# Performance work log

Hardware: AMD Instinct MI355X
Metric: run time of the kernel (lower is better)

Reference implementation:

```python
import jax, jax.numpy as jnp
import numpy as np

N0, N1, N2 = 120000, 30000, 6000   # node frontier sizes per hop
E0, E1 = 480000, 96000             # sampled edges per layer (~fanout 16)
D = 128                            # in_channels == hidden_size
R = 8                              # num_relations
NB = 4                             # num_bases
ETOT = 3000000                     # global edge count (edge_type_all)


def setup_inputs() -> dict:
    key = jax.random.key(0)
    ks = jax.random.split(key, 24)
    s = 1.0 / np.sqrt(D)
    f32 = jnp.float32
    inp = {
        "x": jax.random.normal(ks[0], (N0, D), dtype=f32),
        "src0": jax.random.randint(ks[1], (E0,), 0, N0),
        "dst0": jax.random.randint(ks[2], (E0,), 0, N1),
        "e_id0": jax.random.randint(ks[3], (E0,), 0, ETOT),
        "src1": jax.random.randint(ks[4], (E1,), 0, N1),
        "dst1": jax.random.randint(ks[5], (E1,), 0, N2),
        "e_id1": jax.random.randint(ks[6], (E1,), 0, ETOT),
        "edge_type_all": jax.random.randint(ks[7], (ETOT,), 0, R),
        # pre_layer: linear + relu
        "pre_W": jax.random.normal(ks[8], (D, D), dtype=f32) * s,
        "pre_b": jnp.zeros((D,), f32),
        # RGCNConv layer 0 (basis decomposition)
        "basis0": jax.random.normal(ks[9], (NB, D, D), dtype=f32) * s,
        "comp0": jax.random.normal(ks[10], (R, NB), dtype=f32) * (1.0 / np.sqrt(NB)),
        "root0": jax.random.normal(ks[11], (D, D), dtype=f32) * s,
        "bias0": jnp.zeros((D,), f32),
        "g0": jnp.ones((D,), f32),
        "be0": jnp.zeros((D,), f32),
        # RGCNConv layer 1
        "basis1": jax.random.normal(ks[12], (NB, D, D), dtype=f32) * s,
        "comp1": jax.random.normal(ks[13], (R, NB), dtype=f32) * (1.0 / np.sqrt(NB)),
        "root1": jax.random.normal(ks[14], (D, D), dtype=f32) * s,
        "bias1": jnp.zeros((D,), f32),
        "g1": jnp.ones((D,), f32),
        "be1": jnp.zeros((D,), f32),
        # post_layer: single linear
        "post_W": jax.random.normal(ks[15], (D, D), dtype=f32) * s,
        "post_b": jnp.zeros((D,), f32),
    }
    return inp


def _layernorm(x, g, b, eps=1e-5):
    mu = jnp.mean(x, axis=-1, keepdims=True)
    var = jnp.mean(jnp.square(x - mu), axis=-1, keepdims=True)
    return (x - mu) * jax.lax.rsqrt(var + eps) * g + b


def _rgcn_conv(x, n_dst, src, dst, etype, basis, comp, root, bias):
    # Bipartite RGCNConv with basis decomposition and mean aggregation.
    # Since messages W[r] @ x[src] are linear, aggregate per relation first
    # (segment_sum of raw features), then apply the relation weight once.
    x_t = x[:n_dst]                                    # [n_dst, D]
    out = x_t @ root + bias                            # root/self transform
    W = jnp.einsum('rb,bio->rio', comp, basis)         # [R, D, D]
    x_j = x[src]                                       # [E, D] gather
    deg = jax.ops.segment_sum(jnp.ones(src.shape[0], x.dtype), dst,
                              num_segments=n_dst)      # mean over all relations
    agg = jnp.zeros((n_dst, W.shape[-1]), x.dtype)
    for r in range(W.shape[0]):                        # R=8 structurally distinct
        m = (etype == r).astype(x.dtype)[:, None]
        s_r = jax.ops.segment_sum(x_j * m, dst, num_segments=n_dst)
        agg = agg + s_r @ W[r]
    return out + agg / jnp.maximum(deg, 1.0)[:, None]


def reference(x, src0, dst0, e_id0, src1, dst1, e_id1, edge_type_all,
              pre_W, pre_b, basis0, comp0, root0, bias0, g0, be0,
              basis1, comp1, root1, bias1, g1, be1, post_W, post_b):
    # pre_layer: linear + relu (GeneralMultiLayer, final_act=True)
    h = jax.nn.relu(x @ pre_W + pre_b)
    # layer 0: edge-type gather -> relational conv -> norm -> act (eval: no dropout)
    h = _rgcn_conv(h, N1, src0, dst0, edge_type_all[e_id0],
                   basis0, comp0, root0, bias0)
    h = jax.nn.relu(_layernorm(h, g0, be0))
    # layer 1
    h = _rgcn_conv(h, N2, src1, dst1, edge_type_all[e_id1],
                   basis1, comp1, root1, bias1)
    h = jax.nn.relu(_layernorm(h, g1, be1))
    # post_layer: single linear MLP
    return h @ post_W + post_b
```

## Files before the change

### kernel.cpp

```cpp
#include <hip/hip_runtime.h>
#include <cstdint>

#define DD 128
#define CAP 64
#define ESB 128
#define E0C 480000
#define E1C 96000
#define N0C 120000
#define N1C 30000
#define N2C 6000
#define ETOTC 3000000

typedef unsigned short u16;
typedef __attribute__((ext_vector_type(8))) short bf16x8;
typedef __attribute__((ext_vector_type(16))) float f32x16;

__device__ __forceinline__ u16 f2b(float f) {
    union { float f; unsigned u; } a; a.f = f;
    unsigned r = (a.u + 0x7fffu + ((a.u >> 16) & 1u)) >> 16;
    return (u16)r;
}
__device__ __forceinline__ float b2f(u16 u) {
    union { unsigned u; float f; } a; a.u = ((unsigned)u) << 16;
    return a.f;
}

struct WtJob { const float* src[12]; };
__global__ __launch_bounds__(256) void prep_kernel(
    WtJob job, u16* __restrict__ dst, int* __restrict__ cnt0, int* __restrict__ cnt1,
    const int* __restrict__ etype, unsigned* __restrict__ r4)
{
    int gtid = blockIdx.x * 256 + threadIdx.x;
    for (int i = gtid; i < N1C + N2C; i += 256 * 256) {
        if (i < N1C) cnt0[i] = 0; else cnt1[i - N1C] = 0;
    }
    for (int i = gtid; i < ETOTC / 8; i += 256 * 256) {
        int4 a = ((const int4*)etype)[i * 2];
        int4 b = ((const int4*)etype)[i * 2 + 1];
        unsigned p = (unsigned)(a.x & 7) | ((unsigned)(a.y & 7) << 4)
                   | ((unsigned)(a.z & 7) << 8) | ((unsigned)(a.w & 7) << 12)
                   | ((unsigned)(b.x & 7) << 16) | ((unsigned)(b.y & 7) << 20)
                   | ((unsigned)(b.z & 7) << 24) | ((unsigned)(b.w & 7) << 28);
        r4[i] = p;
    }
    if (blockIdx.x >= 192) return;
    __shared__ float tile[32][33];
    int m = blockIdx.x >> 4;
    int t4 = blockIdx.x & 15;
    int tr = (t4 >> 2) * 32;
    int tc = (t4 & 3) * 32;
    int lx = threadIdx.x & 31, ly = threadIdx.x >> 5;
    #pragma unroll
    for (int yy = 0; yy < 32; yy += 8)
        tile[ly + yy][lx] = job.src[m][(tr + ly + yy) * DD + tc + lx];
    __syncthreads();
    int tid = threadIdx.x;
    if (tid < 128) {
        int nl = tid >> 2, kch = tid & 3;
        int k = tr + kch * 8, n = tc + nl;
        int kc = k >> 4, half = (k >> 3) & 1;
        int t = n >> 5, l31 = n & 31;
        bf16x8 pk;
        #pragma unroll
        for (int j = 0; j < 8; ++j) pk[j] = (short)f2b(tile[kch * 8 + j][nl]);
        *(bf16x8*)(dst + (size_t)m * 16384 + kc * 2048 + t * 512 + half * 256 + l31 * 8) = pk;
    }
}

__global__ __launch_bounds__(256) void fillpre_kernel(
    const float* __restrict__ x,
    const int* __restrict__ src0, const int* __restrict__ dst0, const int* __restrict__ eid0,
    const int* __restrict__ src1, const int* __restrict__ dst1, const int* __restrict__ eid1,
    const unsigned* __restrict__ r4,
    int* __restrict__ cnt0, int* __restrict__ cnt1,
    int* __restrict__ ep0, int* __restrict__ ep1,
    const u16* __restrict__ Wr, const float* __restrict__ bias,
    u16* __restrict__ h0)
{
    if (blockIdx.x < ESB) {
        const int STR = ESB * 256;
        int gtid = blockIdx.x * 256 + threadIdx.x;
        int e = gtid;
        for (; e + 3 * STR < E0C + E1C; e += 4 * STR) {
            int d[4], eidv[4], s[4], r[4], pos[4];
            bool L0[4];
            #pragma unroll
            for (int u = 0; u < 4; ++u) {
                int idx = e + u * STR;
                L0[u] = idx < E0C;
                int ee = L0[u] ? idx : idx - E0C;
                d[u]    = L0[u] ? dst0[ee] : dst1[ee];
                eidv[u] = L0[u] ? eid0[ee] : eid1[ee];
                s[u]    = L0[u] ? src0[ee] : src1[ee];
            }
            #pragma unroll
            for (int u = 0; u < 4; ++u)
                r[u] = (int)((r4[eidv[u] >> 3] >> ((eidv[u] & 7) << 2)) & 7u);
            #pragma unroll
            for (int u = 0; u < 4; ++u)
                pos[u] = atomicAdd(L0[u] ? &cnt0[d[u]] : &cnt1[d[u]], 1);
            #pragma unroll
            for (int u = 0; u < 4; ++u) {
                if (pos[u] < CAP) {
                    int* ep = L0[u] ? ep0 : ep1;
                    ep[(size_t)d[u] * CAP + pos[u]] = s[u] | (r[u] << 28);
                }
            }
        }
        for (; e < E0C + E1C; e += STR) {
            bool L0 = e < E0C;
            int ee = L0 ? e : e - E0C;
            int d   = L0 ? dst0[ee] : dst1[ee];
            int eid = L0 ? eid0[ee] : eid1[ee];
            int s   = L0 ? src0[ee] : src1[ee];
            int r = (int)((r4[eid >> 3] >> ((eid & 7) << 2)) & 7u);
            int pos = atomicAdd(L0 ? &cnt0[d] : &cnt1[d], 1);
            if (pos < CAP) (L0 ? ep0 : ep1)[(size_t)d * CAP + pos] = s | (r << 28);
        }
        return;
    }

    int bid = blockIdx.x - ESB;
    int wave = threadIdx.x >> 6;
    int lane = threadIdx.x & 63;
    int l31 = lane & 31, half = lane >> 5;
    int m0 = (bid * 4 + wave) * 32;
    if (m0 >= N0C) return;
    int arow = m0 + l31;
    bool rv = arow < N0C;

    const float* Aq = x + (size_t)arow * DD;
    float4 st[16];
    if (rv) {
        #pragma unroll
        for (int c = 0; c < 16; ++c)
            st[c] = *(const float4*)(Aq + ((c >> 1) * 16 + half * 8) + (c & 1) * 4);
    } else {
        #pragma unroll
        for (int c = 0; c < 16; ++c) st[c] = make_float4(0.f, 0.f, 0.f, 0.f);
    }
    f32x16 accs[4];
    #pragma unroll
    for (int t = 0; t < 4; ++t)
        #pragma unroll
        for (int i = 0; i < 16; ++i) accs[t][i] = 0.f;
    #pragma unroll
    for (int kc = 0; kc < 8; ++kc) {
        bf16x8 bfr[4];
        #pragma unroll
        for (int t = 0; t < 4; ++t)
            bfr[t] = *(const bf16x8*)(Wr + (size_t)((kc * 4 + t) * 64 + lane) * 8);
        float4 u0 = st[2 * kc], u1 = st[2 * kc + 1];
        bf16x8 af;
        af[0] = (short)f2b(u0.x); af[1] = (short)f2b(u0.y);
        af[2] = (short)f2b(u0.z); af[3] = (short)f2b(u0.w);
        af[4] = (short)f2b(u1.x); af[5] = (short)f2b(u1.y);
        af[6] = (short)f2b(u1.z); af[7] = (short)f2b(u1.w);
        #pragma unroll
        for (int t = 0; t < 4; ++t)
            accs[t] = __builtin_amdgcn_mfma_f32_32x32x16_bf16(af, bfr[t], accs[t], 0, 0, 0);
    }
    float bb[4];
    #pragma unroll
    for (int t = 0; t < 4; ++t) bb[t] = bias[t * 32 + l31];
    #pragma unroll
    for (int reg = 0; reg < 16; ++reg) {
        int rl = (reg & 3) + 8 * (reg >> 2) + 4 * half;
        int row = m0 + rl;
        if (row < N0C) {
            #pragma unroll
            for (int t = 0; t < 4; ++t)
                h0[(size_t)row * DD + t * 32 + l31] =
                    f2b(fmaxf(accs[t][reg] + bb[t], 0.f));
        }
    }
}

__global__ __launch_bounds__(256) void agg_kernel(
    const u16* __restrict__ h, const int* __restrict__ cnt,
    const int* __restrict__ ep, const float* __restrict__ comp,
    u16* __restrict__ T, int ndst)
{
    __shared__ float4 cmp4[8];
    if (threadIdx.x < 8) cmp4[threadIdx.x] = ((const float4*)comp)[threadIdx.x];
    __syncthreads();
    int row = blockIdx.x * 4 + (threadIdx.x >> 6);
    if (row >= ndst) return;
    int lane = threadIdx.x & 63;
    int n = cnt[row];
    int end = n < CAP ? n : CAP;
    const int* erow = ep + (size_t)row * CAP;
    float a0[4] = {0.f, 0.f, 0.f, 0.f};
    float a1[4] = {0.f, 0.f, 0.f, 0.f};
    int j = 0;
    for (; j + 16 <= end; j += 16) {
        int vv[16]; unsigned gg[16];
        #pragma unroll
        for (int u = 0; u < 16; ++u) vv[u] = erow[j + u];
        #pragma unroll
        for (int u = 0; u < 16; ++u)
            gg[u] = *(const unsigned*)(h + (size_t)(vv[u] & 0x0FFFFFFF) * DD + 2 * lane);
        #pragma unroll
        for (int u = 0; u < 16; ++u) {
            float4 c = cmp4[vv[u] >> 28];
            float x0 = b2f((u16)(gg[u] & 0xffffu));
            float x1 = b2f((u16)(gg[u] >> 16));
            a0[0] = fmaf(c.x, x0, a0[0]); a1[0] = fmaf(c.x, x1, a1[0]);
            a0[1] = fmaf(c.y, x0, a0[1]); a1[1] = fmaf(c.y, x1, a1[1]);
            a0[2] = fmaf(c.z, x0, a0[2]); a1[2] = fmaf(c.z, x1, a1[2]);
            a0[3] = fmaf(c.w, x0, a0[3]); a1[3] = fmaf(c.w, x1, a1[3]);
        }
    }
    for (; j + 4 <= end; j += 4) {
        int vv[4]; unsigned gg[4];
        #pragma unroll
        for (int u = 0; u < 4; ++u) vv[u] = erow[j + u];
        #pragma unroll
        for (int u = 0; u < 4; ++u)
            gg[u] = *(const unsigned*)(h + (size_t)(vv[u] & 0x0FFFFFFF) * DD + 2 * lane);
        #pragma unroll
        for (int u = 0; u < 4; ++u) {
            float4 c = cmp4[vv[u] >> 28];
            float x0 = b2f((u16)(gg[u] & 0xffffu));
            float x1 = b2f((u16)(gg[u] >> 16));
            a0[0] = fmaf(c.x, x0, a0[0]); a1[0] = fmaf(c.x, x1, a1[0]);
            a0[1] = fmaf(c.y, x0, a0[1]); a1[1] = fmaf(c.y, x1, a1[1]);
            a0[2] = fmaf(c.z, x0, a0[2]); a1[2] = fmaf(c.z, x1, a1[2]);
            a0[3] = fmaf(c.w, x0, a0[3]); a1[3] = fmaf(c.w, x1, a1[3]);
        }
    }
    for (; j < end; ++j) {
        int v = erow[j];
        unsigned g = *(const unsigned*)(h + (size_t)(v & 0x0FFFFFFF) * DD + 2 * lane);
        float4 c = cmp4[v >> 28];
        float x0 = b2f((u16)(g & 0xffffu));
        float x1 = b2f((u16)(g >> 16));
        a0[0] = fmaf(c.x, x0, a0[0]); a1[0] = fmaf(c.x, x1, a1[0]);
        a0[1] = fmaf(c.y, x0, a0[1]); a1[1] = fmaf(c.y, x1, a1[1]);
        a0[2] = fmaf(c.z, x0, a0[2]); a1[2] = fmaf(c.z, x1, a1[2]);
        a0[3] = fmaf(c.w, x0, a0[3]); a1[3] = fmaf(c.w, x1, a1[3]);
    }
    float inv = 1.f / fmaxf((float)n, 1.f);
    #pragma unroll
    for (int b = 0; b < 4; ++b) {
        unsigned pk = (unsigned)f2b(a0[b] * inv) | ((unsigned)f2b(a1[b] * inv) << 16);
        *(unsigned*)(T + ((size_t)b * ndst + row) * DD + 2 * lane) = pk;
    }
}

__global__ __launch_bounds__(64) void mfma_gemm_ln(
    const u16* __restrict__ Ap, const u16* __restrict__ Ar,
    const u16* __restrict__ Wp, const u16* __restrict__ Wr,
    const float* __restrict__ bias, const float* __restrict__ gw,
    const float* __restrict__ bw, u16* __restrict__ Cv, int nrows)
{
    int lane = threadIdx.x & 63;
    int l31 = lane & 31, half = lane >> 5;
    int m0 = blockIdx.x * 32;
    int arow = m0 + l31;
    bool rv = arow < nrows;
    f32x16 acc[4];
    #pragma unroll
    for (int t = 0; t < 4; ++t)
        #pragma unroll
        for (int i = 0; i < 16; ++i) acc[t][i] = 0.f;

    bf16x8 A0[8], A1[8];
    if (rv) {
        #pragma unroll
        for (int c = 0; c < 8; ++c)
            A0[c] = *(const bf16x8*)(Ap + (size_t)arow * DD + c * 16 + half * 8);
    } else {
        #pragma unroll
        for (int c = 0; c < 8; ++c) A0[c] = (bf16x8){0,0,0,0,0,0,0,0};
    }
    for (int p = 0; p <= 4; ++p) {
        const u16* Wsel = (p == 4) ? Wr : Wp + (size_t)p * 16384;
        if (p < 4) {
            const u16* An = (p + 1 == 4) ? Ar : Ap + (size_t)(p + 1) * nrows * DD;
            if (rv) {
                #pragma unroll
                for (int c = 0; c < 8; ++c)
                    A1[c] = *(const bf16x8*)(An + (size_t)arow * DD + c * 16 + half * 8);
            } else {
                #pragma unroll
                for (int c = 0; c < 8; ++c) A1[c] = (bf16x8){0,0,0,0,0,0,0,0};
            }
        }
        #pragma unroll
        for (int kc = 0; kc < 8; ++kc) {
            bf16x8 bfr[4];
            #pragma unroll
            for (int t = 0; t < 4; ++t)
                bfr[t] = *(const bf16x8*)(Wsel + (size_t)((kc * 4 + t) * 64 + lane) * 8);
            #pragma unroll
            for (int t = 0; t < 4; ++t)
                acc[t] = __builtin_amdgcn_mfma_f32_32x32x16_bf16(A0[kc], bfr[t], acc[t], 0, 0, 0);
        }
        if (p < 4) {
            #pragma unroll
            for (int c = 0; c < 8; ++c) A0[c] = A1[c];
        }
    }

    float bb[4], gg[4], ww[4];
    #pragma unroll
    for (int t = 0; t < 4; ++t) {
        bb[t] = bias[t * 32 + l31];
        gg[t] = gw[t * 32 + l31];
        ww[t] = bw[t * 32 + l31];
    }
    #pragma unroll
    for (int reg = 0; reg < 16; ++reg) {
        int rl = (reg & 3) + 8 * (reg >> 2) + 4 * half;
        int row = m0 + rl;
        float v[4];
        #pragma unroll
        for (int t = 0; t < 4; ++t) v[t] = acc[t][reg] + bb[t];
        float s1 = 0.f, s2 = 0.f;
        #pragma unroll
        for (int t = 0; t < 4; ++t) { s1 += v[t]; s2 += v[t] * v[t]; }
        #pragma unroll
        for (int o = 1; o < 32; o <<= 1) {
            s1 += __shfl_xor(s1, o);
            s2 += __shfl_xor(s2, o);
        }
        float mu = s1 * (1.f / 128.f);
        float var = s2 * (1.f / 128.f) - mu * mu;
        float rstd = rsqrtf(fmaxf(var, 0.f) + 1e-5f);
        if (row < nrows) {
            #pragma unroll
            for (int t = 0; t < 4; ++t)
                Cv[(size_t)row * DD + t * 32 + l31] =
                    f2b(fmaxf((v[t] - mu) * rstd * gg[t] + ww[t], 0.f));
        }
    }
}

__global__ __launch_bounds__(64) void gemm_post_kernel(
    const u16* __restrict__ Ap, const u16* __restrict__ Ar,
    const u16* __restrict__ Wp, const u16* __restrict__ Wr,
    const float* __restrict__ bias, const float* __restrict__ gw,
    const float* __restrict__ bw,
    const u16* __restrict__ Wpost, const float* __restrict__ postb,
    float* __restrict__ outp, int nrows)
{
    __shared__ u16 lt[32][136];
    int lane = threadIdx.x & 63;
    int l31 = lane & 31, half = lane >> 5;
    int m0 = blockIdx.x * 32;
    int arow = m0 + l31;
    bool rv = arow < nrows;
    f32x16 acc[4];
    #pragma unroll
    for (int t = 0; t < 4; ++t)
        #pragma unroll
        for (int i = 0; i < 16; ++i) acc[t][i] = 0.f;

    bf16x8 A0[8], A1[8];
    if (rv) {
        #pragma unroll
        for (int c = 0; c < 8; ++c)
            A0[c] = *(const bf16x8*)(Ap + (size_t)arow * DD + c * 16 + half * 8);
    } else {
        #pragma unroll
        for (int c = 0; c < 8; ++c) A0[c] = (bf16x8){0,0,0,0,0,0,0,0};
    }
    for (int p = 0; p <= 4; ++p) {
        const u16* Wsel = (p == 4) ? Wr : Wp + (size_t)p * 16384;
        if (p < 4) {
            const u16* An = (p + 1 == 4) ? Ar : Ap + (size_t)(p + 1) * nrows * DD;
            if (rv) {
                #pragma unroll
                for (int c = 0; c < 8; ++c)
                    A1[c] = *(const bf16x8*)(An + (size_t)arow * DD + c * 16 + half * 8);
            } else {
                #pragma unroll
                for (int c = 0; c < 8; ++c) A1[c] = (bf16x8){0,0,0,0,0,0,0,0};
            }
        }
        #pragma unroll
        for (int kc = 0; kc < 8; ++kc) {
            bf16x8 bfr[4];
            #pragma unroll
            for (int t = 0; t < 4; ++t)
                bfr[t] = *(const bf16x8*)(Wsel + (size_t)((kc * 4 + t) * 64 + lane) * 8);
            #pragma unroll
            for (int t = 0; t < 4; ++t)
                acc[t] = __builtin_amdgcn_mfma_f32_32x32x16_bf16(A0[kc], bfr[t], acc[t], 0, 0, 0);
        }
        if (p < 4) {
            #pragma unroll
            for (int c = 0; c < 8; ++c) A0[c] = A1[c];
        }
    }

    float bb[4], gg[4], ww[4];
    #pragma unroll
    for (int t = 0; t < 4; ++t) {
        bb[t] = bias[t * 32 + l31];
        gg[t] = gw[t * 32 + l31];
        ww[t] = bw[t * 32 + l31];
    }
    #pragma unroll
    for (int reg = 0; reg < 16; ++reg) {
        int rl = (reg & 3) + 8 * (reg >> 2) + 4 * half;
        float v[4];
        #pragma unroll
        for (int t = 0; t < 4; ++t) v[t] = acc[t][reg] + bb[t];
        float s1 = 0.f, s2 = 0.f;
        #pragma unroll
        for (int t = 0; t < 4; ++t) { s1 += v[t]; s2 += v[t] * v[t]; }
        #pragma unroll
        for (int o = 1; o < 32; o <<= 1) {
            s1 += __shfl_xor(s1, o);
            s2 += __shfl_xor(s2, o);
        }
        float mu = s1 * (1.f / 128.f);
        float var = s2 * (1.f / 128.f) - mu * mu;
        float rstd = rsqrtf(fmaxf(var, 0.f) + 1e-5f);
        #pragma unroll
        for (int t = 0; t < 4; ++t)
            lt[rl][t * 32 + l31] = f2b(fmaxf((v[t] - mu) * rstd * gg[t] + ww[t], 0.f));
    }
    __syncthreads();

    f32x16 acc2[4];
    #pragma unroll
    for (int t = 0; t < 4; ++t)
        #pragma unroll
        for (int i = 0; i < 16; ++i) acc2[t][i] = 0.f;
    bf16x8 A[8];
    #pragma unroll
    for (int c = 0; c < 8; ++c)
        A[c] = *(const bf16x8*)&lt[l31][c * 16 + half * 8];
    #pragma unroll
    for (int kc = 0; kc < 8; ++kc) {
        bf16x8 bfr[4];
        #pragma unroll
        for (int t = 0; t < 4; ++t)
            bfr[t] = *(const bf16x8*)(Wpost + (size_t)((kc * 4 + t) * 64 + lane) * 8);
        #pragma unroll
        for (int t = 0; t < 4; ++t)
            acc2[t] = __builtin_amdgcn_mfma_f32_32x32x16_bf16(A[kc], bfr[t], acc2[t], 0, 0, 0);
    }
    float pb[4];
    #pragma unroll
    for (int t = 0; t < 4; ++t) pb[t] = postb[t * 32 + l31];
    #pragma unroll
    for (int reg = 0; reg < 16; ++reg) {
        int rl = (reg & 3) + 8 * (reg >> 2) + 4 * half;
        int row = m0 + rl;
        if (row < nrows) {
            #pragma unroll
            for (int t = 0; t < 4; ++t)
                outp[(size_t)row * DD + t * 32 + l31] = acc2[t][reg] + pb[t];
        }
    }
}

extern "C" void kernel_launch(void* const* d_in, const int* in_sizes, int n_in,
                              void* d_out, int out_size, void* d_ws, size_t ws_size,
                              hipStream_t stream)
{
    const float* x     = (const float*)d_in[0];
    const int* src0    = (const int*)d_in[1];
    const int* dst0    = (const int*)d_in[2];
    const int* eid0    = (const int*)d_in[3];
    const int* src1    = (const int*)d_in[4];
    const int* dst1    = (const int*)d_in[5];
    const int* eid1    = (const int*)d_in[6];
    const int* etype   = (const int*)d_in[7];
    const float* preW  = (const float*)d_in[8];
    const float* preb  = (const float*)d_in[9];
    const float* basis0 = (const float*)d_in[10];
    const float* comp0  = (const float*)d_in[11];
    const float* root0  = (const float*)d_in[12];
    const float* bias0  = (const float*)d_in[13];
    const float* g0    = (const float*)d_in[14];
    const float* be0   = (const float*)d_in[15];
    const float* basis1 = (const float*)d_in[16];
    const float* comp1  = (const float*)d_in[17];
    const float* root1  = (const float*)d_in[18];
    const float* bias1  = (const float*)d_in[19];
    const float* g1    = (const float*)d_in[20];
    const float* be1   = (const float*)d_in[21];
    const float* postW = (const float*)d_in[22];
    const float* postb = (const float*)d_in[23];
    float* out = (float*)d_out;

    char* ws = (char*)d_ws;
    size_t o = 0;
    auto alloc = [&](size_t bytes) { char* p = ws + o; o += (bytes + 255) & ~(size_t)255; return p; };
    u16* h0   = (u16*)alloc((size_t)N0C * DD * 2);
    u16* T0   = (u16*)alloc((size_t)4 * N1C * DD * 2);
    u16* h1   = (u16*)alloc((size_t)N1C * DD * 2);
    u16* T1   = (u16*)alloc((size_t)4 * N2C * DD * 2);
    u16* wt   = (u16*)alloc((size_t)12 * 16384 * 2);
    int* cnt0 = (int*)alloc((size_t)N1C * 4);
    int* cnt1 = (int*)alloc((size_t)N2C * 4);
    int* ep0  = (int*)alloc((size_t)N1C * CAP * 4);
    int* ep1  = (int*)alloc((size_t)N2C * CAP * 4);
    unsigned* r4 = (unsigned*)alloc((size_t)(ETOTC / 8) * 4);

    WtJob job;
    job.src[0] = preW;
    for (int b = 0; b < 4; ++b) job.src[1 + b] = basis0 + (size_t)b * 16384;
    job.src[5] = root0;
    for (int b = 0; b < 4; ++b) job.src[6 + b] = basis1 + (size_t)b * 16384;
    job.src[10] = root1;
    job.src[11] = postW;

    prep_kernel<<<256, 256, 0, stream>>>(job, wt, cnt0, cnt1, etype, r4);
    fillpre_kernel<<<ESB + (N0C + 127) / 128, 256, 0, stream>>>(
        x, src0, dst0, eid0, src1, dst1, eid1, r4,
        cnt0, cnt1, ep0, ep1, wt + 0 * 16384, preb, h0);
    agg_kernel<<<(N1C + 3) / 4, 256, 0, stream>>>(h0, cnt0, ep0, comp0, T0, N1C);
    mfma_gemm_ln<<<(N1C + 31) / 32, 64, 0, stream>>>(
        T0, h0, wt + 1 * 16384, wt + 5 * 16384, bias0, g0, be0, h1, N1C);
    agg_kernel<<<(N2C + 3) / 4, 256, 0, stream>>>(h1, cnt1, ep1, comp1, T1, N2C);
    gemm_post_kernel<<<(N2C + 31) / 32, 64, 0, stream>>>(
        T1, h1, wt + 6 * 16384, wt + 10 * 16384, bias1, g1, be1,
        wt + 11 * 16384, postb, out, N2C);
}
```

Measured before the change: 274.1 us.

## Fuse the five post-prep stages into one cooperative persistent kernel with grid syncs

Replaces the fillpre, two aggregation and two GEMM launches with a single cooperative kernel of 512 blocks that runs each stage as a grid-strided loop, separated by grid-wide syncs. It targets launch overhead and tail gaps between the dependent stages. In exchange it imposes a fixed grid size on every stage, which may underuse the GPU in the gather-heavy aggregation. It also adds grid barrier costs and replaces a __syncthreads with a waitcnt for the per-wave LDS tile. The original multi-kernel path is kept as a fallback if the cooperative launch fails.

```diff
diff --git a/kernel.cpp b/kernel.cpp
--- a/kernel.cpp
+++ b/kernel.cpp
@@ -1,15 +1,21 @@
 #include <hip/hip_runtime.h>
+#include <hip/hip_cooperative_groups.h>
 #include <cstdint>
+
+namespace cg = cooperative_groups;
 
 #define DD 128
 #define CAP 64
 #define ESB 128
+#define MESB 256
 #define E0C 480000
 #define E1C 96000
 #define N0C 120000
 #define N1C 30000
 #define N2C 6000
 #define ETOTC 3000000
+#define MGB 512
+#define MGW (MGB * 4)
 
 typedef unsigned short u16;
 typedef __attribute__((ext_vector_type(8))) short bf16x8;
@@ -67,78 +73,67 @@
     }
 }
 
-__global__ __launch_bounds__(256) void fillpre_kernel(
-    const float* __restrict__ x,
+
+__device__ __forceinline__ void fill_edges(
+    int nblocks, int blockid,
     const int* __restrict__ src0, const int* __restrict__ dst0, const int* __restrict__ eid0,
     const int* __restrict__ src1, const int* __restrict__ dst1, const int* __restrict__ eid1,
     const unsigned* __restrict__ r4,
     int* __restrict__ cnt0, int* __restrict__ cnt1,
-    int* __restrict__ ep0, int* __restrict__ ep1,
-    const u16* __restrict__ Wr, const float* __restrict__ bias,
-    u16* __restrict__ h0)
-{
-    if (blockIdx.x < ESB) {
-        const int STR = ESB * 256;
-        int gtid = blockIdx.x * 256 + threadIdx.x;
-        int e = gtid;
-        for (; e + 3 * STR < E0C + E1C; e += 4 * STR) {
-            int d[4], eidv[4], s[4], r[4], pos[4];
-            bool L0[4];
-            #pragma unroll
-            for (int u = 0; u < 4; ++u) {
-                int idx = e + u * STR;
-                L0[u] = idx < E0C;
-                int ee = L0[u] ? idx : idx - E0C;
-                d[u]    = L0[u] ? dst0[ee] : dst1[ee];
-                eidv[u] = L0[u] ? eid0[ee] : eid1[ee];
-                s[u]    = L0[u] ? src0[ee] : src1[ee];
+    int* __restrict__ ep0, int* __restrict__ ep1)
+{
+    const int STR = nblocks * 256;
+    int gtid = blockid * 256 + threadIdx.x;
+    int e = gtid;
+    for (; e + 3 * STR < E0C + E1C; e += 4 * STR) {
+        int d[4], eidv[4], s[4], r[4], pos[4];
+        bool L0[4];
+        #pragma unroll
+        for (int u = 0; u < 4; ++u) {
+            int idx = e + u * STR;
+            L0[u] = idx < E0C;
+            int ee = L0[u] ? idx : idx - E0C;
+            d[u]    = L0[u] ? dst0[ee] : dst1[ee];
+            eidv[u] = L0[u] ? eid0[ee] : eid1[ee];
+            s[u]    = L0[u] ? src0[ee] : src1[ee];
+        }
+        #pragma unroll
+        for (int u = 0; u < 4; ++u)
+            r[u] = (int)((r4[eidv[u] >> 3] >> ((eidv[u] & 7) << 2)) & 7u);
+        #pragma unroll
+        for (int u = 0; u < 4; ++u)
+            pos[u] = atomicAdd(L0[u] ? &cnt0[d[u]] : &cnt1[d[u]], 1);
+        #pragma unroll
+        for (int u = 0; u < 4; ++u) {
+            if (pos[u] < CAP) {
+                int* ep = L0[u] ? ep0 : ep1;
+                ep[(size_t)d[u] * CAP + pos[u]] = s[u] | (r[u] << 28);
             }
-            #pragma unroll
-            for (int u = 0; u < 4; ++u)
-                r[u] = (int)((r4[eidv[u] >> 3] >> ((eidv[u] & 7) << 2)) & 7u);
-            #pragma unroll
-            for (int u = 0; u < 4; ++u)
-                pos[u] = atomicAdd(L0[u] ? &cnt0[d[u]] : &cnt1[d[u]], 1);
-            #pragma unroll
-            for (int u = 0; u < 4; ++u) {
-                if (pos[u] < CAP) {
-                    int* ep = L0[u] ? ep0 : ep1;
-                    ep[(size_t)d[u] * CAP + pos[u]] = s[u] | (r[u] << 28);
-                }
-            }
-        }
-        for (; e < E0C + E1C; e += STR) {
-            bool L0 = e < E0C;
-            int ee = L0 ? e : e - E0C;
-            int d   = L0 ? dst0[ee] : dst1[ee];
-            int eid = L0 ? eid0[ee] : eid1[ee];
-            int s   = L0 ? src0[ee] : src1[ee];
-            int r = (int)((r4[eid >> 3] >> ((eid & 7) << 2)) & 7u);
-            int pos = atomicAdd(L0 ? &cnt0[d] : &cnt1[d], 1);
-            if (pos < CAP) (L0 ? ep0 : ep1)[(size_t)d * CAP + pos] = s | (r << 28);
-        }
-        return;
-    }
-
-    int bid = blockIdx.x - ESB;
-    int wave = threadIdx.x >> 6;
-    int lane = threadIdx.x & 63;
+        }
+    }
+    for (; e < E0C + E1C; e += STR) {
+        bool L0 = e < E0C;
+        int ee = L0 ? e : e - E0C;
+        int d   = L0 ? dst0[ee] : dst1[ee];
+        int eid = L0 ? eid0[ee] : eid1[ee];
+        int s   = L0 ? src0[ee] : src1[ee];
+        int r = (int)((r4[eid >> 3] >> ((eid & 7) << 2)) & 7u);
+        int pos = atomicAdd(L0 ? &cnt0[d] : &cnt1[d], 1);
+        if (pos < CAP) (L0 ? ep0 : ep1)[(size_t)d * CAP + pos] = s | (r << 28);
+    }
+}
+
+__device__ __forceinline__ void pre_tile(
+    const float* __restrict__ x, const u16* __restrict__ Wr,
+    const float* __restrict__ bias, u16* __restrict__ h0, int m0, int lane)
+{
     int l31 = lane & 31, half = lane >> 5;
-    int m0 = (bid * 4 + wave) * 32;
-    if (m0 >= N0C) return;
     int arow = m0 + l31;
-    bool rv = arow < N0C;
-
     const float* Aq = x + (size_t)arow * DD;
     float4 st[16];
-    if (rv) {
-        #pragma unroll
-        for (int c = 0; c < 16; ++c)
-            st[c] = *(const float4*)(Aq + ((c >> 1) * 16 + half * 8) + (c & 1) * 4);
-    } else {
-        #pragma unroll
-        for (int c = 0; c < 16; ++c) st[c] = make_float4(0.f, 0.f, 0.f, 0.f);
-    }
+    #pragma unroll
+    for (int c = 0; c < 16; ++c)
+        st[c] = *(const float4*)(Aq + ((c >> 1) * 16 + half * 8) + (c & 1) * 4);
     f32x16 accs[4];
     #pragma unroll
     for (int t = 0; t < 4; ++t)
@@ -167,26 +162,17 @@
     for (int reg = 0; reg < 16; ++reg) {
         int rl = (reg & 3) + 8 * (reg >> 2) + 4 * half;
         int row = m0 + rl;
-        if (row < N0C) {
-            #pragma unroll
-            for (int t = 0; t < 4; ++t)
-                h0[(size_t)row * DD + t * 32 + l31] =
-                    f2b(fmaxf(accs[t][reg] + bb[t], 0.f));
-        }
-    }
-}
-
-__global__ __launch_bounds__(256) void agg_kernel(
+        #pragma unroll
+        for (int t = 0; t < 4; ++t)
+            h0[(size_t)row * DD + t * 32 + l31] = f2b(fmaxf(accs[t][reg] + bb[t], 0.f));
+    }
+}
+
+__device__ __forceinline__ void agg_row(
     const u16* __restrict__ h, const int* __restrict__ cnt,
-    const int* __restrict__ ep, const float* __restrict__ comp,
-    u16* __restrict__ T, int ndst)
-{
-    __shared__ float4 cmp4[8];
-    if (threadIdx.x < 8) cmp4[threadIdx.x] = ((const float4*)comp)[threadIdx.x];
-    __syncthreads();
-    int row = blockIdx.x * 4 + (threadIdx.x >> 6);
-    if (row >= ndst) return;
-    int lane = threadIdx.x & 63;
+    const int* __restrict__ ep, const float4* cmp4,
+    u16* __restrict__ T, int ndst, int row, int lane)
+{
     int n = cnt[row];
     int end = n < CAP ? n : CAP;
     const int* erow = ep + (size_t)row * CAP;
@@ -248,23 +234,18 @@
     }
 }
 
-__global__ __launch_bounds__(64) void mfma_gemm_ln(
+__device__ __forceinline__ void conv_tile_acc(
     const u16* __restrict__ Ap, const u16* __restrict__ Ar,
     const u16* __restrict__ Wp, const u16* __restrict__ Wr,
-    const float* __restrict__ bias, const float* __restrict__ gw,
-    const float* __restrict__ bw, u16* __restrict__ Cv, int nrows)
-{
-    int lane = threadIdx.x & 63;
+    int nrows, int m0, int lane, f32x16 acc[4])
+{
     int l31 = lane & 31, half = lane >> 5;
-    int m0 = blockIdx.x * 32;
     int arow = m0 + l31;
     bool rv = arow < nrows;
-    f32x16 acc[4];
     #pragma unroll
     for (int t = 0; t < 4; ++t)
         #pragma unroll
         for (int i = 0; i < 16; ++i) acc[t][i] = 0.f;
-
     bf16x8 A0[8], A1[8];
     if (rv) {
         #pragma unroll
@@ -302,13 +283,23 @@
             for (int c = 0; c < 8; ++c) A0[c] = A1[c];
         }
     }
-
+}
+
+__device__ __forceinline__ void gemm_ln_tile(
+    const u16* __restrict__ Ap, const u16* __restrict__ Ar,
+    const u16* __restrict__ Wp, const u16* __restrict__ Wr,
+    const float* __restrict__ bias, const float* __restrict__ gwp,
+    const float* __restrict__ bwp, u16* __restrict__ Cv, int nrows, int m0, int lane)
+{
+    int l31 = lane & 31, half = lane >> 5;
+    f32x16 acc[4];
+    conv_tile_acc(Ap, Ar, Wp, Wr, nrows, m0, lane, acc);
     float bb[4], gg[4], ww[4];
     #pragma unroll
     for (int t = 0; t < 4; ++t) {
         bb[t] = bias[t * 32 + l31];
-        gg[t] = gw[t * 32 + l31];
-        ww[t] = bw[t * 32 + l31];
+        gg[t] = gwp[t * 32 + l31];
+        ww[t] = bwp[t * 32 + l31];
     }
     #pragma unroll
     for (int reg = 0; reg < 16; ++reg) {
@@ -337,6 +328,181 @@
     }
 }
 
+__device__ __forceinline__ void gemm_post_tile(
+    const u16* __restrict__ Ap, const u16* __restrict__ Ar,
+    const u16* __restrict__ Wp, const u16* __restrict__ Wr,
+    const float* __restrict__ bias, const float* __restrict__ gwp,
+    const float* __restrict__ bwp,
+    const u16* __restrict__ Wpost, const float* __restrict__ postb,
+    float* __restrict__ outp, int nrows, int m0, int lane, u16 (*lt)[136])
+{
+    int l31 = lane & 31, half = lane >> 5;
+    f32x16 acc[4];
+    conv_tile_acc(Ap, Ar, Wp, Wr, nrows, m0, lane, acc);
+    float bb[4], gg[4], ww[4];
+    #pragma unroll
+    for (int t = 0; t < 4; ++t) {
+        bb[t] = bias[t * 32 + l31];
+        gg[t] = gwp[t * 32 + l31];
+        ww[t] = bwp[t * 32 + l31];
+    }
+    #pragma unroll
+    for (int reg = 0; reg < 16; ++reg) {
+        int rl = (reg & 3) + 8 * (reg >> 2) + 4 * half;
+        float v[4];
+        #pragma unroll
+        for (int t = 0; t < 4; ++t) v[t] = acc[t][reg] + bb[t];
+        float s1 = 0.f, s2 = 0.f;
+        #pragma unroll
+        for (int t = 0; t < 4; ++t) { s1 += v[t]; s2 += v[t] * v[t]; }
+        #pragma unroll
+        for (int o = 1; o < 32; o <<= 1) {
+            s1 += __shfl_xor(s1, o);
+            s2 += __shfl_xor(s2, o);
+        }
+        float mu = s1 * (1.f / 128.f);
+        float var = s2 * (1.f / 128.f) - mu * mu;
+        float rstd = rsqrtf(fmaxf(var, 0.f) + 1e-5f);
+        #pragma unroll
+        for (int t = 0; t < 4; ++t)
+            lt[rl][t * 32 + l31] = f2b(fmaxf((v[t] - mu) * rstd * gg[t] + ww[t], 0.f));
+    }
+    asm volatile("s_waitcnt lgkmcnt(0)" ::: "memory");
+    __builtin_amdgcn_sched_barrier(0);
+
+    f32x16 acc2[4];
+    #pragma unroll
+    for (int t = 0; t < 4; ++t)
+        #pragma unroll
+        for (int i = 0; i < 16; ++i) acc2[t][i] = 0.f;
+    bf16x8 A[8];
+    #pragma unroll
+    for (int c = 0; c < 8; ++c)
+        A[c] = *(const bf16x8*)&lt[l31][c * 16 + half * 8];
+    #pragma unroll
+    for (int kc = 0; kc < 8; ++kc) {
+        bf16x8 bfr[4];
+        #pragma unroll
+        for (int t = 0; t < 4; ++t)
+            bfr[t] = *(const bf16x8*)(Wpost + (size_t)((kc * 4 + t) * 64 + lane) * 8);
+        #pragma unroll
+        for (int t = 0; t < 4; ++t)
+            acc2[t] = __builtin_amdgcn_mfma_f32_32x32x16_bf16(A[kc], bfr[t], acc2[t], 0, 0, 0);
+    }
+    float pb[4];
+    #pragma unroll
+    for (int t = 0; t < 4; ++t) pb[t] = postb[t * 32 + l31];
+    #pragma unroll
+    for (int reg = 0; reg < 16; ++reg) {
+        int rl = (reg & 3) + 8 * (reg >> 2) + 4 * half;
+        int row = m0 + rl;
+        if (row < nrows) {
+            #pragma unroll
+            for (int t = 0; t < 4; ++t)
+                outp[(size_t)row * DD + t * 32 + l31] = acc2[t][reg] + pb[t];
+        }
+    }
+}
+
+struct MegaArgs {
+    const float* x;
+    const int *src0, *dst0, *eid0, *src1, *dst1, *eid1;
+    const unsigned* r4;
+    int *cnt0, *cnt1, *ep0, *ep1;
+    const u16* wt;
+    const float *preb, *comp0, *comp1;
+    const float *bias0, *g0, *be0, *bias1, *g1, *be1, *postb;
+    u16 *h0, *T0, *h1, *T1;
+    float* outp;
+};
+
+__global__ __launch_bounds__(256, 2) void mega_kernel(MegaArgs a)
+{
+    cg::grid_group grid = cg::this_grid();
+    __shared__ float4 c0s[8], c1s[8];
+    __shared__ u16 lt[4][32][136];
+    if (threadIdx.x < 8) c0s[threadIdx.x] = ((const float4*)a.comp0)[threadIdx.x];
+    else if (threadIdx.x < 16) c1s[threadIdx.x - 8] = ((const float4*)a.comp1)[threadIdx.x - 8];
+    __syncthreads();
+
+    int wave = threadIdx.x >> 6, lane = threadIdx.x & 63;
+    int wid = blockIdx.x * 4 + wave;
+
+    if (blockIdx.x < MESB) {
+        fill_edges(MESB, blockIdx.x, a.src0, a.dst0, a.eid0, a.src1, a.dst1, a.eid1,
+                   a.r4, a.cnt0, a.cnt1, a.ep0, a.ep1);
+    } else {
+        int gw = (blockIdx.x - MESB) * 4 + wave;
+        for (int t = gw; t < N0C / 32; t += (MGB - MESB) * 4)
+            pre_tile(a.x, a.wt, a.preb, a.h0, t * 32, lane);
+    }
+    grid.sync();
+
+    for (int row = wid; row < N1C; row += MGW)
+        agg_row(a.h0, a.cnt0, a.ep0, c0s, a.T0, N1C, row, lane);
+    grid.sync();
+
+    for (int t = wid; t < (N1C + 31) / 32; t += MGW)
+        gemm_ln_tile(a.T0, a.h0, a.wt + 1 * 16384, a.wt + 5 * 16384,
+                     a.bias0, a.g0, a.be0, a.h1, N1C, t * 32, lane);
+    grid.sync();
+
+    for (int row = wid; row < N2C; row += MGW)
+        agg_row(a.h1, a.cnt1, a.ep1, c1s, a.T1, N2C, row, lane);
+    grid.sync();
+
+    for (int t = wid; t < (N2C + 31) / 32; t += MGW)
+        gemm_post_tile(a.T1, a.h1, a.wt + 6 * 16384, a.wt + 10 * 16384,
+                       a.bias1, a.g1, a.be1, a.wt + 11 * 16384, a.postb,
+                       a.outp, N2C, t * 32, lane, lt[wave]);
+}
+
+
+__global__ __launch_bounds__(256) void fillpre_kernel(
+    const float* __restrict__ x,
+    const int* __restrict__ src0, const int* __restrict__ dst0, const int* __restrict__ eid0,
+    const int* __restrict__ src1, const int* __restrict__ dst1, const int* __restrict__ eid1,
+    const unsigned* __restrict__ r4,
+    int* __restrict__ cnt0, int* __restrict__ cnt1,
+    int* __restrict__ ep0, int* __restrict__ ep1,
+    const u16* __restrict__ Wr, const float* __restrict__ bias,
+    u16* __restrict__ h0)
+{
+    if (blockIdx.x < ESB) {
+        fill_edges(ESB, blockIdx.x, src0, dst0, eid0, src1, dst1, eid1,
+                   r4, cnt0, cnt1, ep0, ep1);
+        return;
+    }
+    int bid = blockIdx.x - ESB;
+    int wave = threadIdx.x >> 6, lane = threadIdx.x & 63;
+    int m0 = (bid * 4 + wave) * 32;
+    if (m0 >= N0C) return;
+    pre_tile(x, Wr, bias, h0, m0, lane);
+}
+
+__global__ __launch_bounds__(256) void agg_kernel(
+    const u16* __restrict__ h, const int* __restrict__ cnt,
+    const int* __restrict__ ep, const float* __restrict__ comp,
+    u16* __restrict__ T, int ndst)
+{
+    __shared__ float4 cmp4[8];
+    if (threadIdx.x < 8) cmp4[threadIdx.x] = ((const float4*)comp)[threadIdx.x];
+    __syncthreads();
+    int row = blockIdx.x * 4 + (threadIdx.x >> 6);
+    if (row >= ndst) return;
+    agg_row(h, cnt, ep, cmp4, T, ndst, row, threadIdx.x & 63);
+}
+
+__global__ __launch_bounds__(64) void mfma_gemm_ln(
+    const u16* __restrict__ Ap, const u16* __restrict__ Ar,
+    const u16* __restrict__ Wp, const u16* __restrict__ Wr,
+    const float* __restrict__ bias, const float* __restrict__ gw,
+    const float* __restrict__ bw, u16* __restrict__ Cv, int nrows)
+{
+    gemm_ln_tile(Ap, Ar, Wp, Wr, bias, gw, bw, Cv, nrows,
+                 blockIdx.x * 32, threadIdx.x & 63);
+}
+
 __global__ __launch_bounds__(64) void gemm_post_kernel(
     const u16* __restrict__ Ap, const u16* __restrict__ Ar,
     const u16* __restrict__ Wp, const u16* __restrict__ Wr,
@@ -346,117 +512,8 @@
     float* __restrict__ outp, int nrows)
 {
     __shared__ u16 lt[32][136];
-    int lane = threadIdx.x & 63;
-    int l31 = lane & 31, half = lane >> 5;
-    int m0 = blockIdx.x * 32;
-    int arow = m0 + l31;
-    bool rv = arow < nrows;
-    f32x16 acc[4];
-    #pragma unroll
-    for (int t = 0; t < 4; ++t)
-        #pragma unroll
-        for (int i = 0; i < 16; ++i) acc[t][i] = 0.f;
-
-    bf16x8 A0[8], A1[8];
-    if (rv) {
-        #pragma unroll
-        for (int c = 0; c < 8; ++c)
-            A0[c] = *(const bf16x8*)(Ap + (size_t)arow * DD + c * 16 + half * 8);
-    } else {
-        #pragma unroll
-        for (int c = 0; c < 8; ++c) A0[c] = (bf16x8){0,0,0,0,0,0,0,0};
-    }
-    for (int p = 0; p <= 4; ++p) {
-        const u16* Wsel = (p == 4) ? Wr : Wp + (size_t)p * 16384;
-        if (p < 4) {
-            const u16* An = (p + 1 == 4) ? Ar : Ap + (size_t)(p + 1) * nrows * DD;
-            if (rv) {
-                #pragma unroll
-                for (int c = 0; c < 8; ++c)
-                    A1[c] = *(const bf16x8*)(An + (size_t)arow * DD + c * 16 + half * 8);
-            } else {
-                #pragma unroll
-                for (int c = 0; c < 8; ++c) A1[c] = (bf16x8){0,0,0,0,0,0,0,0};
-            }
-        }
-        #pragma unroll
-        for (int kc = 0; kc < 8; ++kc) {
-            bf16x8 bfr[4];
-            #pragma unroll
-            for (int t = 0; t < 4; ++t)
-                bfr[t] = *(const bf16x8*)(Wsel + (size_t)((kc * 4 + t) * 64 + lane) * 8);
-            #pragma unroll
-            for (int t = 0; t < 4; ++t)
-                acc[t] = __builtin_amdgcn_mfma_f32_32x32x16_bf16(A0[kc], bfr[t], acc[t], 0, 0, 0);
-        }
-        if (p < 4) {
-            #pragma unroll
-            for (int c = 0; c < 8; ++c) A0[c] = A1[c];
-        }
-    }
-
-    float bb[4], gg[4], ww[4];
-    #pragma unroll
-    for (int t = 0; t < 4; ++t) {
-        bb[t] = bias[t * 32 + l31];
-        gg[t] = gw[t * 32 + l31];
-        ww[t] = bw[t * 32 + l31];
-    }
-    #pragma unroll
-    for (int reg = 0; reg < 16; ++reg) {
-        int rl = (reg & 3) + 8 * (reg >> 2) + 4 * half;
-        float v[4];
-        #pragma unroll
-        for (int t = 0; t < 4; ++t) v[t] = acc[t][reg] + bb[t];
-        float s1 = 0.f, s2 = 0.f;
-        #pragma unroll
-        for (int t = 0; t < 4; ++t) { s1 += v[t]; s2 += v[t] * v[t]; }
-        #pragma unroll
-        for (int o = 1; o < 32; o <<= 1) {
-            s1 += __shfl_xor(s1, o);
-            s2 += __shfl_xor(s2, o);
-        }
-        float mu = s1 * (1.f / 128.f);
-        float var = s2 * (1.f / 128.f) - mu * mu;
-        float rstd = rsqrtf(fmaxf(var, 0.f) + 1e-5f);
-        #pragma unroll
-        for (int t = 0; t < 4; ++t)
-            lt[rl][t * 32 + l31] = f2b(fmaxf((v[t] - mu) * rstd * gg[t] + ww[t], 0.f));
-    }
-    __syncthreads();
-
-    f32x16 acc2[4];
-    #pragma unroll
-    for (int t = 0; t < 4; ++t)
-        #pragma unroll
-        for (int i = 0; i < 16; ++i) acc2[t][i] = 0.f;
-    bf16x8 A[8];
-    #pragma unroll
-    for (int c = 0; c < 8; ++c)
-        A[c] = *(const bf16x8*)&lt[l31][c * 16 + half * 8];
-    #pragma unroll
-    for (int kc = 0; kc < 8; ++kc) {
-        bf16x8 bfr[4];
-        #pragma unroll
-        for (int t = 0; t < 4; ++t)
-            bfr[t] = *(const bf16x8*)(Wpost + (size_t)((kc * 4 + t) * 64 + lane) * 8);
-        #pragma unroll
-        for (int t = 0; t < 4; ++t)
-            acc2[t] = __builtin_amdgcn_mfma_f32_32x32x16_bf16(A[kc], bfr[t], acc2[t], 0, 0, 0);
-    }
-    float pb[4];
-    #pragma unroll
-    for (int t = 0; t < 4; ++t) pb[t] = postb[t * 32 + l31];
-    #pragma unroll
-    for (int reg = 0; reg < 16; ++reg) {
-        int rl = (reg & 3) + 8 * (reg >> 2) + 4 * half;
-        int row = m0 + rl;
-        if (row < nrows) {
-            #pragma unroll
-            for (int t = 0; t < 4; ++t)
-                outp[(size_t)row * DD + t * 32 + l31] = acc2[t][reg] + pb[t];
-        }
-    }
+    gemm_post_tile(Ap, Ar, Wp, Wr, bias, gw, bw, Wpost, postb, outp, nrows,
+                   blockIdx.x * 32, threadIdx.x & 63, lt);
 }
 
 extern "C" void kernel_launch(void* const* d_in, const int* in_sizes, int n_in,
@@ -512,14 +569,33 @@
     job.src[11] = postW;
 
     prep_kernel<<<256, 256, 0, stream>>>(job, wt, cnt0, cnt1, etype, r4);
-    fillpre_kernel<<<ESB + (N0C + 127) / 128, 256, 0, stream>>>(
-        x, src0, dst0, eid0, src1, dst1, eid1, r4,
-        cnt0, cnt1, ep0, ep1, wt + 0 * 16384, preb, h0);
-    agg_kernel<<<(N1C + 3) / 4, 256, 0, stream>>>(h0, cnt0, ep0, comp0, T0, N1C);
-    mfma_gemm_ln<<<(N1C + 31) / 32, 64, 0, stream>>>(
-        T0, h0, wt + 1 * 16384, wt + 5 * 16384, bias0, g0, be0, h1, N1C);
-    agg_kernel<<<(N2C + 3) / 4, 256, 0, stream>>>(h1, cnt1, ep1, comp1, T1, N2C);
-    gemm_post_kernel<<<(N2C + 31) / 32, 64, 0, stream>>>(
-        T1, h1, wt + 6 * 16384, wt + 10 * 16384, bias1, g1, be1,
-        wt + 11 * 16384, postb, out, N2C);
-}
+
+    MegaArgs ma;
+    ma.x = x;
+    ma.src0 = src0; ma.dst0 = dst0; ma.eid0 = eid0;
+    ma.src1 = src1; ma.dst1 = dst1; ma.eid1 = eid1;
+    ma.r4 = r4;
+    ma.cnt0 = cnt0; ma.cnt1 = cnt1; ma.ep0 = ep0; ma.ep1 = ep1;
+    ma.wt = wt;
+    ma.preb = preb; ma.comp0 = comp0; ma.comp1 = comp1;
+    ma.bias0 = bias0; ma.g0 = g0; ma.be0 = be0;
+    ma.bias1 = bias1; ma.g1 = g1; ma.be1 = be1;
+    ma.postb = postb;
+    ma.h0 = h0; ma.T0 = T0; ma.h1 = h1; ma.T1 = T1;
+    ma.outp = out;
+    void* kargs[] = { &ma };
+    hipError_t cerr = hipLaunchCooperativeKernel((void*)mega_kernel, dim3(MGB),
+                                                 dim3(256), kargs, 0, stream);
+    if (cerr != hipSuccess) {
+        fillpre_kernel<<<ESB + (N0C + 127) / 128, 256, 0, stream>>>(
+            x, src0, dst0, eid0, src1, dst1, eid1, r4,
+            cnt0, cnt1, ep0, ep1, wt + 0 * 16384, preb, h0);
+        agg_kernel<<<(N1C + 3) / 4, 256, 0, stream>>>(h0, cnt0, ep0, comp0, T0, N1C);
+        mfma_gemm_ln<<<(N1C + 31) / 32, 64, 0, stream>>>(
+            T0, h0, wt + 1 * 16384, wt + 5 * 16384, bias0, g0, be0, h1, N1C);
+        agg_kernel<<<(N2C + 3) / 4, 256, 0, stream>>>(h1, cnt1, ep1, comp1, T1, N2C);
+        gemm_post_kernel<<<(N2C + 31) / 32, 64, 0, stream>>>(
+            T1, h1, wt + 6 * 16384, wt + 10 * 16384, bias1, g1, be1,
+            wt + 11 * 16384, postb, out, N2C);
+    }
+}
```

Result: slower. 713.1 us (+160.2%).
